# Performance work log

Hardware: AMD Instinct MI355X
Metric: run time of the kernel (lower is better)

The kernel has to match this reference:

```python
import jax, jax.numpy as jnp
import numpy as np

SIGMA_MAX = 0.15
SIGMA_MIN = 0.001
# AutoNCP(16, 1): inter=9, command=6, motor=1.  (fan_in, hidden) per NCP layer:
LAYERS = [(4, 9), (9, 6), (6, 1)]
B, T, IN = 4096, 512, 4


def setup_inputs() -> dict:
    rng = np.random.default_rng(0)
    inp = {"x": jnp.asarray(rng.standard_normal((B, T, IN)), dtype=jnp.float32)}
    for l, (fin, hid) in enumerate(LAYERS):
        cat = fin + hid
        s = 1.0 / np.sqrt(cat)
        for nm in ("ff1", "ff2", "ta", "tb"):
            inp[f"{nm}_w{l}"] = jnp.asarray(rng.uniform(-s, s, (hid, cat)), dtype=jnp.float32)
            inp[f"{nm}_b{l}"] = jnp.asarray(rng.uniform(-s, s, (hid,)), dtype=jnp.float32)
        m_in = (rng.random((hid, fin)) < 0.5).astype(np.float32)
        m_in[m_in.sum(axis=1) == 0, 0] = 1.0  # ensure every neuron has >=1 input synapse
        inp[f"mask{l}"] = jnp.asarray(np.concatenate([m_in, np.ones((hid, hid), np.float32)], axis=1))
    inp["sigma_scale"] = jnp.asarray([SIGMA_MAX - SIGMA_MIN], dtype=jnp.float32)
    return inp


def _cfc_cell(xx, w1, b1, w2, b2, wa, ba, wb, bb, mask):
    # xx: [B, fan_in + hidden]; ff1/ff2 are sparsity-masked, time gates are dense
    ff1 = jnp.tanh(xx @ (w1 * mask).T + b1)
    ff2 = jnp.tanh(xx @ (w2 * mask).T + b2)
    t_interp = jax.nn.sigmoid(xx @ wa.T + ba + xx @ wb.T + bb)  # ts = 1.0
    return ff1 * (1.0 - t_interp) + t_interp * ff2


def _cfc_forward(x, params, masks):
    b = x.shape[0]

    def step(hs, xt):
        inp = xt
        new_hs = []
        for p, m, h in zip(params, masks, hs):
            h_new = _cfc_cell(jnp.concatenate([inp, h], axis=1), *p, m)
            new_hs.append(h_new)
            inp = h_new  # feed-forward through inter -> command -> motor
        return tuple(new_hs), inp

    init = tuple(jnp.zeros((b, hid), x.dtype) for _, hid in LAYERS)
    final_hs, outs = jax.lax.scan(step, init, jnp.swapaxes(x, 0, 1))
    return jnp.swapaxes(outs, 0, 1), jnp.concatenate(final_hs, axis=1)  # [B,T,1], [B,16]


def reference(x,
              ff1_w0, ff1_b0, ff2_w0, ff2_b0, ta_w0, ta_b0, tb_w0, tb_b0, mask0,
              ff1_w1, ff1_b1, ff2_w1, ff2_b1, ta_w1, ta_b1, tb_w1, tb_b1, mask1,
              ff1_w2, ff1_b2, ff2_w2, ff2_b2, ta_w2, ta_b2, tb_w2, tb_b2, mask2,
              sigma_scale):
    params = [
        (ff1_w0, ff1_b0, ff2_w0, ff2_b0, ta_w0, ta_b0, tb_w0, tb_b0),
        (ff1_w1, ff1_b1, ff2_w1, ff2_b1, ta_w1, ta_b1, tb_w1, tb_b1),
        (ff1_w2, ff1_b2, ff2_w2, ff2_b2, ta_w2, ta_b2, tb_w2, tb_b2),
    ]
    out, hx = _cfc_forward(x, params, [mask0, mask1, mask2])
    sigma = jax.nn.sigmoid(out) * sigma_scale + SIGMA_MIN
    return (sigma, hx)
```

## Files before the change

### kernel.cpp

```cpp
#include <hip/hip_runtime.h>


#define LOG2E 1.44269504088896340736f
#define SMIN  0.001f

static constexpr int BATCH = 4096;
static constexpr int TLEN  = 512;

__device__ __forceinline__ float frcp(float x)  { return __builtin_amdgcn_rcpf(x); }
__device__ __forceinline__ float fexp2(float x) { return __builtin_amdgcn_exp2f(x); }
template<int CTRL>
__device__ __forceinline__ float dppf(float v) {
    return __int_as_float(__builtin_amdgcn_update_dpp(
        0, __float_as_int(v), CTRL, 0xF, 0xF, true));
}

#define ROTSTEP(CTRL, R) { const float vr = dppf<CTRL>(F);                               \
    if ((R) & 1) { a0b = fmaf(w0r[R], vr, a0b); a1b = fmaf(w1r[R], vr, a1b);             \
                   a2b = fmaf(w2r[R], vr, a2b); }                                        \
    else         { a0  = fmaf(w0r[R], vr, a0 ); a1  = fmaf(w1r[R], vr, a1 );             \
                   a2  = fmaf(w2r[R], vr, a2 ); } }

struct Params { const float* p[29]; float* out; };

__global__ __launch_bounds__(256, 1) void cfc_kernel(Params P) {
    const int tid = threadIdx.x;
    const int li  = tid & 15;
    const int e   = (blockIdx.x << 4) + (tid >> 4);

    const float got = dppf<0x121>((float)li);
    const int   dir = (((int)got) == ((li + 1) & 15)) ? 1 : -1;

    const int role = (li <= 8) ? 0 : (li <= 14 ? 1 : 2);
    const int jn   = (role == 0) ? li : (role == 1 ? li - 9 : 0);

    const float *Wf1, *Bf1, *Wf2, *Bf2, *Wa, *Ba, *Wb, *Bb, *Mk;
    int cat;
    if (role == 0)      { Wf1=P.p[1];  Bf1=P.p[2];  Wf2=P.p[3];  Bf2=P.p[4];
                          Wa=P.p[5];   Ba=P.p[6];   Wb=P.p[7];   Bb=P.p[8];  Mk=P.p[9];  cat=13; }
    else if (role == 1) { Wf1=P.p[10]; Bf1=P.p[11]; Wf2=P.p[12]; Bf2=P.p[13];
                          Wa=P.p[14];  Ba=P.p[15];  Wb=P.p[16];  Bb=P.p[17]; Mk=P.p[18]; cat=15; }
    else                { Wf1=P.p[19]; Bf1=P.p[20]; Wf2=P.p[21]; Bf2=P.p[22];
                          Wa=P.p[23];  Ba=P.p[24];  Wb=P.p[25];  Bb=P.p[26]; Mk=P.p[27]; cat=7;  }

    const float sc01 = -2.0f * LOG2E, sc2 = -LOG2E;
    float b0 = sc01 * Bf1[jn], b1 = sc01 * Wf2[0] * 0.f + sc01 * Bf2[jn], b2 = sc2 * (Ba[jn] + Bb[jn]);

    float xw0[4], xw1[4], xw2[4];
    #pragma unroll
    for (int c = 0; c < 4; ++c) {
        float a = 0.f, bq = 0.f, cq = 0.f;
        if (role == 0) {
            const int idx = jn * 13 + c;
            const float m = Mk[idx];
            a  = sc01 * Wf1[idx] * m;
            bq = sc01 * Wf2[idx] * m;
            cq = sc2  * (Wa[idx] + Wb[idx]);
        }
        xw0[c] = a; xw1[c] = bq; xw2[c] = cq;
    }

    float w0r[16], w1r[16], w2r[16];
    #pragma unroll
    for (int r = 0; r < 16; ++r) {
        const int k = (li + dir * r) & 15;
        int cc = -1;
        if (role == 0)      { if (k <= 8)  cc = 4 + k; }
        else if (role == 1) { if (k <= 14) cc = k; }
        else                { if (k >= 9)  cc = (k == 15) ? 6 : (k - 9); }
        float a = 0.f, bq = 0.f, cq = 0.f;
        if (cc >= 0) {
            const int idx = jn * cat + cc;
            const float m = Mk[idx];
            a  = sc01 * Wf1[idx] * m;
            bq = sc01 * Wf2[idx] * m;
            cq = sc2  * (Wa[idx] + Wb[idx]);
        }
        w0r[r] = a  + a;  b0 -= a;
        w1r[r] = bq + bq; b1 -= bq;
        w2r[r] = cq + cq; b2 -= cq;
    }

    const float sig_scale = P.p[28][0];

    float F   = 0.5f;
    float sgv = 0.f;

    const float4* xp = reinterpret_cast<const float4*>(P.p[0]) + (size_t)e * TLEN;
    float* op = P.out + (size_t)e * TLEN;

    auto STEP = [&](const float4 xv, bool cA, bool cB, bool cC) {
        sgv = fmaf(sig_scale, frcp(1.0f + fexp2(fmaf(-2.0f * LOG2E, F, LOG2E))), SMIN);
        float a0 = b0, a1 = b1, a2 = b2;
        float a0b = xw0[0] * xv.x, a1b = xw1[0] * xv.x, a2b = xw2[0] * xv.x;
        a0b = fmaf(xw0[1], xv.y, a0b); a1b = fmaf(xw1[1], xv.y, a1b); a2b = fmaf(xw2[1], xv.y, a2b);
        a0b = fmaf(xw0[2], xv.z, a0b); a1b = fmaf(xw1[2], xv.z, a1b); a2b = fmaf(xw2[2], xv.z, a2b);
        a0b = fmaf(xw0[3], xv.w, a0b); a1b = fmaf(xw1[3], xv.w, a1b); a2b = fmaf(xw2[3], xv.w, a2b);
        a0 = fmaf(w0r[0], F, a0); a1 = fmaf(w1r[0], F, a1); a2 = fmaf(w2r[0], F, a2);
        ROTSTEP(0x121, 1)  ROTSTEP(0x122, 2)  ROTSTEP(0x123, 3)  ROTSTEP(0x124, 4)
        ROTSTEP(0x125, 5)  ROTSTEP(0x126, 6)  ROTSTEP(0x127, 7)  ROTSTEP(0x128, 8)
        ROTSTEP(0x129, 9)  ROTSTEP(0x12A, 10) ROTSTEP(0x12B, 11) ROTSTEP(0x12C, 12)
        ROTSTEP(0x12D, 13) ROTSTEP(0x12E, 14) ROTSTEP(0x12F, 15)
        const float y0 = a0 + a0b, y1 = a1 + a1b, y2 = a2 + a2b;
        const float f0 = frcp(1.0f + fexp2(y0));
        const float f1 = frcp(1.0f + fexp2(y1));
        const float f2 = frcp(1.0f + fexp2(y2));
        const float Fn = fmaf(f2, f1 - f0, f0);
        const bool cm = (role == 0) ? cA : ((role == 1) ? cB : cC);
        F = cm ? Fn : F;
    };

    STEP(xp[0], true, false, false);
    STEP(xp[1], true, true,  false);
    STEP(xp[2], true, true,  true);

    float4 xs0 = xp[3], xs1 = xp[4], xs2 = xp[5], xs3 = xp[6];
    for (int m = 0; m < 127; ++m) {
        const int t = 3 + 4 * m;
        int pn = t + 4; if (pn > 508) pn = 508;
        const float4 xn0 = xp[pn], xn1 = xp[pn + 1], xn2 = xp[pn + 2], xn3 = xp[pn + 3];
        STEP(xs0, true, true, true); const float s0 = sgv;
        STEP(xs1, true, true, true); const float s1 = sgv;
        STEP(xs2, true, true, true); const float s2 = sgv;
        STEP(xs3, true, true, true); const float s3 = sgv;
        if (li == 15) { op[t - 3] = s0; op[t - 2] = s1; op[t - 1] = s2; op[t] = s3; }
        xs0 = xn0; xs1 = xn1; xs2 = xn2; xs3 = xn3;
    }
    STEP(xs3, true, true, true);  const float s508 = sgv;

    STEP(xs3, false, true,  true);  const float s509 = sgv;
    STEP(xs3, false, false, true);  const float s510 = sgv;
    STEP(xs3, false, false, false); const float s511 = sgv;
    if (li == 15) { op[508] = s508; op[509] = s509; op[510] = s510; op[511] = s511; }

    P.out[(size_t)BATCH * TLEN + (size_t)e * 16 + li] = fmaf(2.0f, F, -1.0f);
}

extern "C" void kernel_launch(void* const* d_in, const int* in_sizes, int n_in,
                              void* d_out, int out_size, void* d_ws, size_t ws_size,
                              hipStream_t stream) {
    (void)in_sizes; (void)n_in; (void)out_size; (void)d_ws; (void)ws_size;
    Params P;
    for (int i = 0; i < 29; ++i) P.p[i] = (const float*)d_in[i];
    P.out = (float*)d_out;
    hipLaunchKernelGGL(cfc_kernel, dim3(BATCH / 16), dim3(256), 0, stream, P);
}
```

Measured before the change: 92.56 us.

## Split each CfC sequence across 32 lanes with permlane16 swap reduction

Each batch element now uses 32 lanes instead of 16. Each half-row handles half of the rotated recurrent terms and half of the input features, and the two partial sums are combined with permlane16_swap (falling back to ds_swizzle). The change shortens the serial FMA chain per timestep on the latency-bound recurrence, and launch bounds allow two blocks per CU. In exchange it doubles the thread count, adds cross-row swaps and a DPP rotate per step, and halves the number of elements handled per block.

```diff
diff --git a/kernel.cpp b/kernel.cpp
--- a/kernel.cpp
+++ b/kernel.cpp
@@ -15,24 +15,49 @@
         0, __float_as_int(v), CTRL, 0xF, 0xF, true));
 }
 
-#define ROTSTEP(CTRL, R) { const float vr = dppf<CTRL>(F);                               \
-    if ((R) & 1) { a0b = fmaf(w0r[R], vr, a0b); a1b = fmaf(w1r[R], vr, a1b);             \
-                   a2b = fmaf(w2r[R], vr, a2b); }                                        \
-    else         { a0  = fmaf(w0r[R], vr, a0 ); a1  = fmaf(w1r[R], vr, a1 );             \
-                   a2  = fmaf(w2r[R], vr, a2 ); } }
+#if defined(__has_builtin)
+#if __has_builtin(__builtin_amdgcn_permlane16_swap)
+#define HAVE_PL16 1
+#endif
+#endif
+
+__device__ __forceinline__ void pswap(float v, float& o0, float& o1) {
+#ifdef HAVE_PL16
+    auto r = __builtin_amdgcn_permlane16_swap(__float_as_uint(v),
+                                              __float_as_uint(v), false, false);
+    o0 = __uint_as_float(r[0]);
+    o1 = __uint_as_float(r[1]);
+#else
+    const float s = __int_as_float(
+        __builtin_amdgcn_ds_swizzle(__float_as_int(v), 0x401F));
+    o0 = s; o1 = s;
+#endif
+}
+
+#define ROTSTEP(CTRL, R) { const float vr = dppf<CTRL>(F);      \
+    a0 = fmaf(w0r[R], vr, a0); a1 = fmaf(w1r[R], vr, a1);       \
+    a2 = fmaf(w2r[R], vr, a2); }
 
 struct Params { const float* p[29]; float* out; };
 
-__global__ __launch_bounds__(256, 1) void cfc_kernel(Params P) {
+__global__ __launch_bounds__(256, 2) void cfc_kernel(Params P) {
     const int tid = threadIdx.x;
-    const int li  = tid & 15;
-    const int e   = (blockIdx.x << 4) + (tid >> 4);
+    const int lie = tid & 31;
+    const int li  = lie & 15;
+    const int h   = lie >> 4;
+    const int e   = ((blockIdx.x << 8) + tid) >> 5;
 
     const float got = dppf<0x121>((float)li);
     const int   dir = (((int)got) == ((li + 1) & 15)) ? 1 : -1;
 
+    float p0, p1;
+    pswap((float)(tid & 63), p0, p1);
+    const bool useP0 = (((int)p0) == ((tid & 63) ^ 16));
+
     const int role = (li <= 8) ? 0 : (li <= 14 ? 1 : 2);
     const int jn   = (role == 0) ? li : (role == 1 ? li - 9 : 0);
+    const int ns   = (li + 8 * h) & 15;
+    const int srole = (ns <= 8) ? 0 : (ns <= 14 ? 1 : 2);
 
     const float *Wf1, *Bf1, *Wf2, *Bf2, *Wa, *Ba, *Wb, *Bb, *Mk;
     int cat;
@@ -44,14 +69,20 @@
                           Wa=P.p[23];  Ba=P.p[24];  Wb=P.p[25];  Bb=P.p[26]; Mk=P.p[27]; cat=7;  }
 
     const float sc01 = -2.0f * LOG2E, sc2 = -LOG2E;
-    float b0 = sc01 * Bf1[jn], b1 = sc01 * Wf2[0] * 0.f + sc01 * Bf2[jn], b2 = sc2 * (Ba[jn] + Bb[jn]);
 
-    float xw0[4], xw1[4], xw2[4];
+    float b0 = 0.f, b1 = 0.f, b2 = 0.f;
+    if (h == 0) {
+        b0 = sc01 * Bf1[jn];
+        b1 = sc01 * Bf2[jn];
+        b2 = sc2  * (Ba[jn] + Bb[jn]);
+    }
+
+    float xw0[2], xw1[2], xw2[2];
     #pragma unroll
-    for (int c = 0; c < 4; ++c) {
+    for (int c = 0; c < 2; ++c) {
         float a = 0.f, bq = 0.f, cq = 0.f;
         if (role == 0) {
-            const int idx = jn * 13 + c;
+            const int idx = jn * 13 + 2 * h + c;
             const float m = Mk[idx];
             a  = sc01 * Wf1[idx] * m;
             bq = sc01 * Wf2[idx] * m;
@@ -60,10 +91,10 @@
         xw0[c] = a; xw1[c] = bq; xw2[c] = cq;
     }
 
-    float w0r[16], w1r[16], w2r[16];
+    float w0r[8], w1r[8], w2r[8];
     #pragma unroll
-    for (int r = 0; r < 16; ++r) {
-        const int k = (li + dir * r) & 15;
+    for (int r = 0; r < 8; ++r) {
+        const int k = (li + dir * (8 * h + r)) & 15;
         int cc = -1;
         if (role == 0)      { if (k <= 8)  cc = 4 + k; }
         else if (role == 1) { if (k <= 14) cc = k; }
@@ -91,22 +122,26 @@
 
     auto STEP = [&](const float4 xv, bool cA, bool cB, bool cC) {
         sgv = fmaf(sig_scale, frcp(1.0f + fexp2(fmaf(-2.0f * LOG2E, F, LOG2E))), SMIN);
-        float a0 = b0, a1 = b1, a2 = b2;
-        float a0b = xw0[0] * xv.x, a1b = xw1[0] * xv.x, a2b = xw2[0] * xv.x;
-        a0b = fmaf(xw0[1], xv.y, a0b); a1b = fmaf(xw1[1], xv.y, a1b); a2b = fmaf(xw2[1], xv.y, a2b);
-        a0b = fmaf(xw0[2], xv.z, a0b); a1b = fmaf(xw1[2], xv.z, a1b); a2b = fmaf(xw2[2], xv.z, a2b);
-        a0b = fmaf(xw0[3], xv.w, a0b); a1b = fmaf(xw1[3], xv.w, a1b); a2b = fmaf(xw2[3], xv.w, a2b);
-        a0 = fmaf(w0r[0], F, a0); a1 = fmaf(w1r[0], F, a1); a2 = fmaf(w2r[0], F, a2);
-        ROTSTEP(0x121, 1)  ROTSTEP(0x122, 2)  ROTSTEP(0x123, 3)  ROTSTEP(0x124, 4)
-        ROTSTEP(0x125, 5)  ROTSTEP(0x126, 6)  ROTSTEP(0x127, 7)  ROTSTEP(0x128, 8)
-        ROTSTEP(0x129, 9)  ROTSTEP(0x12A, 10) ROTSTEP(0x12B, 11) ROTSTEP(0x12C, 12)
-        ROTSTEP(0x12D, 13) ROTSTEP(0x12E, 14) ROTSTEP(0x12F, 15)
-        const float y0 = a0 + a0b, y1 = a1 + a1b, y2 = a2 + a2b;
-        const float f0 = frcp(1.0f + fexp2(y0));
-        const float f1 = frcp(1.0f + fexp2(y1));
-        const float f2 = frcp(1.0f + fexp2(y2));
-        const float Fn = fmaf(f2, f1 - f0, f0);
-        const bool cm = (role == 0) ? cA : ((role == 1) ? cB : cC);
+        const float xc0 = h ? xv.z : xv.x;
+        const float xc1 = h ? xv.w : xv.y;
+        float a0 = fmaf(xw0[0], xc0, b0);
+        float a1 = fmaf(xw1[0], xc0, b1);
+        float a2 = fmaf(xw2[0], xc0, b2);
+        a0 = fmaf(xw0[1], xc1, a0); a1 = fmaf(xw1[1], xc1, a1); a2 = fmaf(xw2[1], xc1, a2);
+        a0 = fmaf(w0r[0], F, a0);   a1 = fmaf(w1r[0], F, a1);   a2 = fmaf(w2r[0], F, a2);
+        ROTSTEP(0x121, 1) ROTSTEP(0x122, 2) ROTSTEP(0x123, 3) ROTSTEP(0x124, 4)
+        ROTSTEP(0x125, 5) ROTSTEP(0x126, 6) ROTSTEP(0x127, 7)
+        float u0, u1;
+        pswap(a0, u0, u1); a0 += useP0 ? u0 : u1;
+        pswap(a1, u0, u1); a1 += useP0 ? u0 : u1;
+        pswap(a2, u0, u1); a2 += useP0 ? u0 : u1;
+        const float f0 = frcp(1.0f + fexp2(a0));
+        const float f1 = frcp(1.0f + fexp2(a1));
+        const float f2 = frcp(1.0f + fexp2(a2));
+        float Fn = fmaf(f2, f1 - f0, f0);
+        const float Fr = dppf<0x128>(Fn);
+        Fn = h ? Fr : Fn;
+        const bool cm = (srole == 0) ? cA : ((srole == 1) ? cB : cC);
         F = cm ? Fn : F;
     };
 
@@ -123,7 +158,7 @@
         STEP(xs1, true, true, true); const float s1 = sgv;
         STEP(xs2, true, true, true); const float s2 = sgv;
         STEP(xs3, true, true, true); const float s3 = sgv;
-        if (li == 15) { op[t - 3] = s0; op[t - 2] = s1; op[t - 1] = s2; op[t] = s3; }
+        if (lie == 15) { op[t - 3] = s0; op[t - 2] = s1; op[t - 1] = s2; op[t] = s3; }
         xs0 = xn0; xs1 = xn1; xs2 = xn2; xs3 = xn3;
     }
     STEP(xs3, true, true, true);  const float s508 = sgv;
@@ -131,9 +166,10 @@
     STEP(xs3, false, true,  true);  const float s509 = sgv;
     STEP(xs3, false, false, true);  const float s510 = sgv;
     STEP(xs3, false, false, false); const float s511 = sgv;
-    if (li == 15) { op[508] = s508; op[509] = s509; op[510] = s510; op[511] = s511; }
+    if (lie == 15) { op[508] = s508; op[509] = s509; op[510] = s510; op[511] = s511; }
 
-    P.out[(size_t)BATCH * TLEN + (size_t)e * 16 + li] = fmaf(2.0f, F, -1.0f);
+    if (h == 0)
+        P.out[(size_t)BATCH * TLEN + (size_t)e * 16 + li] = fmaf(2.0f, F, -1.0f);
 }
 
 extern "C" void kernel_launch(void* const* d_in, const int* in_sizes, int n_in,
@@ -143,5 +179,5 @@
     Params P;
     for (int i = 0; i < 29; ++i) P.p[i] = (const float*)d_in[i];
     P.out = (float*)d_out;
-    hipLaunchKernelGGL(cfc_kernel, dim3(BATCH / 16), dim3(256), 0, stream, P);
+    hipLaunchKernelGGL(cfc_kernel, dim3(BATCH / 8), dim3(256), 0, stream, P);
 }
```

New measurement: 177.9 us. 92.2% more time.
